# Optimization experiments

Measured on AMD Instinct MI355X. Metric: run time of the kernel, lower is better.

## Reference

```python
import jax, jax.numpy as jnp
import numpy as np
import math

DIM = 1024
D_IN = 2048      # expand * dim
N = 16           # d_state
NG = 32          # ngroups
DT_RANK = 64     # ceil(dim/16)
D_CONV = 4
B, L = 2, 1024


def setup_inputs() -> dict:
    key = jax.random.key(0)
    ks = jax.random.split(key, 10)
    nrm = lambda k, shp, s: jax.random.normal(k, shp, jnp.float32) * s
    x = jax.random.normal(ks[0], (B, L, DIM), jnp.float32)
    latent = jnp.zeros((B, NG, D_IN, N), jnp.float32)
    W_in = nrm(ks[1], (2 * D_IN, DIM), 0.02)          # in_proj (no bias)
    conv_w = nrm(ks[2], (D_IN, 1, D_CONV), 0.1)        # depthwise conv weight
    conv_b = nrm(ks[3], (D_IN,), 0.02)                 # conv bias
    W_x = nrm(ks[4], (DT_RANK + 2 * N, D_IN), 0.02)    # x_proj (no bias)
    W_dt = nrm(ks[5], (D_IN, DT_RANK), 0.02)           # dt_proj weight
    b_dt = nrm(ks[6], (D_IN,), 0.1)                    # dt_proj bias
    W_out = nrm(ks[7], (DIM, D_IN), 0.02)              # out_proj (no bias)
    A_log = jnp.log(jnp.tile(jnp.arange(1, N + 1, dtype=jnp.float32), (D_IN, 1)))
    D = jnp.ones((D_IN,), jnp.float32)
    W_cattn = nrm(ks[8], (3 * N, N), 0.02)             # c_attn (no bias)
    return dict(x=x, latent=latent, W_in=W_in, conv_w=conv_w, conv_b=conv_b,
                W_x=W_x, W_dt=W_dt, b_dt=b_dt, W_out=W_out, A_log=A_log,
                D=D, W_cattn=W_cattn)


def _scan_op(e1, e2):
    a1, b1 = e1
    a2, b2 = e2
    return a2 * a1, a2 * b1 + b2


def reference(x, latent, W_in, conv_w, conv_b, W_x, W_dt, b_dt, W_out, A_log, D, W_cattn):
    b, l, _ = x.shape
    xr = x @ W_in.T                                  # [b,l,2*d_in]
    u, res = xr[..., :D_IN], xr[..., D_IN:]
    # depthwise causal conv1d (padding d_conv-1 then truncate to l == left-pad)
    uc = jnp.transpose(u, (0, 2, 1))                 # [b,d_in,l]
    uc = jax.lax.conv_general_dilated(
        uc, conv_w, window_strides=(1,), padding=[(D_CONV - 1, 0)],
        feature_group_count=D_IN, dimension_numbers=('NCH', 'OIH', 'NCH'))
    uc = uc + conv_b[None, :, None]
    u = jax.nn.silu(jnp.transpose(uc, (0, 2, 1)))    # [b,l,d_in]

    A = -jnp.exp(A_log)                              # [d_in,n]
    x_dbl = u @ W_x.T                                # [b,l,dt_rank+2n]
    delta = jax.nn.softplus(x_dbl[..., :DT_RANK] @ W_dt.T + b_dt)  # [b,l,d_in]
    Bm = x_dbl[..., DT_RANK:DT_RANK + N]             # [b,l,n]
    Cm = x_dbl[..., DT_RANK + N:]                    # [b,l,n]

    dA = jnp.exp(delta[..., None] * A)               # [b,l,d_in,n]
    dBu = delta[..., None] * Bm[:, :, None, :] * u[..., None]  # [b,l,d_in,n]

    pg = l // NG
    dA = dA.reshape(b, NG, pg, D_IN, N)
    dBu = dBu.reshape(b, NG, pg, D_IN, N)
    Cg = Cm.reshape(b, NG, pg, N)
    dBu = dBu.at[:, :, 0].add(latent)                # inject group latent

    # parallel scan of h_t = dA_t * h_{t-1} + dBu_t within each group
    _, hs = jax.lax.associative_scan(_scan_op, (dA, dBu), axis=2)
    y = jnp.einsum('bgpdn,bgpn->bgpd', hs, Cg).reshape(b, l, D_IN)
    y = y + u * D

    # latent communication: causal attention over group latents (initial latent, per source)
    qkv = latent[:, :-1] @ W_cattn.T                 # [b,ng-1,d_in,3n]
    q, k, v = jnp.split(qkv, 3, axis=-1)
    G = NG - 1
    q = q.reshape(b, G, -1)
    k = k.reshape(b, G, -1)
    v = v.reshape(b, G, -1)
    scale = 1.0 / math.sqrt(D_IN * N)
    scores = (q @ jnp.swapaxes(k, 1, 2)) * scale     # [b,G,G]
    mask = jnp.tril(jnp.ones((G, G), bool))
    scores = jnp.where(mask, scores, -jnp.inf)
    attn = jax.nn.softmax(scores, axis=-1)
    lat = (attn @ v).reshape(b, G, D_IN, N)
    lat_out = jnp.concatenate([jnp.zeros((b, 1, D_IN, N), x.dtype), lat], axis=1)

    out = (y * jax.nn.silu(res)) @ W_out.T           # [b,l,dim]
    return out, lat_out
```

## Files before the change

kernel.cpp:

```cpp
#include <hip/hip_runtime.h>
#include <stdint.h>

typedef uint16_t u16;
typedef u16   u16x4  __attribute__((ext_vector_type(4)));
typedef u16   u16x8  __attribute__((ext_vector_type(8)));
typedef __bf16 bf16x8 __attribute__((ext_vector_type(8)));
typedef float f32x4  __attribute__((ext_vector_type(4)));

__device__ __forceinline__ float b2f(u16 x) {
    union { uint32_t u; float f; } c; c.u = ((uint32_t)x) << 16; return c.f;
}
__device__ __forceinline__ u16 f2b(float f) {
    union { float f; uint32_t u; } c; c.f = f;
    uint32_t r = c.u + 0x7FFFu + ((c.u >> 16) & 1u);
    return (u16)(r >> 16);
}
__device__ __forceinline__ float silu_f(float x) { return x / (1.f + __expf(-x)); }
__device__ __forceinline__ float softplus_f(float x) {
    return fmaxf(x, 0.f) + __logf(1.f + __expf(-fabsf(x)));
}

__device__ __forceinline__ void gload16(const u16* g, u16* l) {
    __builtin_amdgcn_global_load_lds(
        (const __attribute__((address_space(1))) void*)(g),
        (__attribute__((address_space(3))) void*)(l), 16, 0, 0);
}

__device__ __forceinline__ int dtype_flag_block(const u16* __restrict__ xraw) {
    __shared__ int bad;
    if (threadIdx.x == 0) bad = 0;
    __syncthreads();
    float v = b2f(xraw[threadIdx.x]);
    if (!(fabsf(v) < 1000.f)) atomicAdd(&bad, 1);
    __syncthreads();
    return bad;
}

struct CvtArgs {
    const void* s[13];
    u16* d[13];
    int cum[14];
    int total;
};
__global__ __launch_bounds__(256) void cvt_all_k(CvtArgs a, const u16* __restrict__ xraw)
{
    int flag = dtype_flag_block(xraw);
    int u4 = blockIdx.x * 256 + threadIdx.x;
    if (u4 >= a.total) return;
    int seg = 0;
    while (u4 >= a.cum[seg + 1]) seg++;
    int local = u4 - a.cum[seg];
    const void* s = a.s[seg];
    u16x4 o;
    if (s == nullptr) {
        o[0] = o[1] = o[2] = o[3] = 0;
    } else if (flag) {
        f32x4 vv = ((const f32x4*)s)[local];
        for (int e = 0; e < 4; e++) o[e] = f2b(vv[e]);
    } else {
        o = ((const u16x4*)s)[local];
    }
    *(u16x4*)(a.d[seg] + (size_t)local * 4) = o;
}

template<int EPI, int TN>
__device__ __forceinline__ void gemm_core(
    int bx, int by, int bz,
    const u16* __restrict__ A, const u16* __restrict__ B,
    int Kc, int lda, int ldb,
    u16* __restrict__ Cb, float* __restrict__ Cf, int ldc, int ncols,
    size_t zslab)
{
    constexpr int NJ = TN / 32;
    constexpr int BT = TN / 32;
    __shared__ __align__(16) u16 lA[128 * 64];
    __shared__ __align__(16) u16 lB[TN * 64];
    const int tid  = threadIdx.x;
    const int wave = tid >> 6, lane = tid & 63;
    const int quad = lane >> 4, l16 = lane & 15;
    const int wm = wave & 1, wn = wave >> 1;
    const int row0 = by * 128, col0 = bx * TN;
    const int kbeg = bz * Kc;

    f32x4 acc[4][NJ];
    const f32x4 zf = {0.f, 0.f, 0.f, 0.f};
    for (int i = 0; i < 4; i++) for (int j = 0; j < NJ; j++) acc[i][j] = zf;

    const u16* Ap[4]; const u16* Bp[BT];
    int lbaseA[4], lbaseB[BT];
    for (int t = 0; t < 4; t++) {
        int c = t * 256 + tid;
        int r = c >> 3, s = c & 7;
        int q = (s - (r >> 1)) & 7;
        Ap[t] = A + (size_t)(row0 + r) * lda + q * 8 + kbeg;
        lbaseA[t] = (t * 256 + wave * 64) * 8;
    }
    for (int t = 0; t < BT; t++) {
        int c = t * 256 + tid;
        int r = c >> 3, s = c & 7;
        int q = (s - (r >> 1)) & 7;
        Bp[t] = B + (size_t)(col0 + r) * ldb + q * 8 + kbeg;
        lbaseB[t] = (t * 256 + wave * 64) * 8;
    }

    for (int k0 = 0; k0 < Kc; k0 += 64) {
        for (int t = 0; t < 4; t++) gload16(Ap[t] + k0, &lA[lbaseA[t]]);
        for (int t = 0; t < BT; t++) gload16(Bp[t] + k0, &lB[lbaseB[t]]);
        __syncthreads();
        for (int half = 0; half < 2; half++) {
            bf16x8 af[4], bfr[NJ];
            for (int i = 0; i < 4; i++) {
                int r = wm * 64 + i * 16 + l16;
                int s = (half * 4 + quad + (r >> 1)) & 7;
                af[i] = *(const bf16x8*)&lA[r * 64 + s * 8];
            }
            for (int j = 0; j < NJ; j++) {
                int r = wn * (TN / 2) + j * 16 + l16;
                int s = (half * 4 + quad + (r >> 1)) & 7;
                bfr[j] = *(const bf16x8*)&lB[r * 64 + s * 8];
            }
            for (int i = 0; i < 4; i++)
                for (int j = 0; j < NJ; j++)
                    acc[i][j] = __builtin_amdgcn_mfma_f32_16x16x32_bf16(af[i], bfr[j], acc[i][j], 0, 0, 0);
        }
        __syncthreads();
    }

    float* dstf = (EPI == 2) ? (Cf + (size_t)bz * zslab) : Cf;
    for (int i = 0; i < 4; i++) {
        int mb = row0 + wm * 64 + i * 16 + quad * 4;
        for (int j = 0; j < NJ; j++) {
            int n = col0 + wn * (TN / 2) + j * 16 + l16;
            if (n >= ncols) continue;
            if (EPI == 0) {
                for (int v = 0; v < 4; v++)
                    Cb[(size_t)(mb + v) * ldc + n] = f2b(acc[i][j][v]);
            } else {
                for (int v = 0; v < 4; v++)
                    dstf[(size_t)(mb + v) * ldc + n] = acc[i][j][v];
            }
        }
    }
}

template<int EPI, int TN>
__global__ __launch_bounds__(256) void gemm_bt(
    const u16* __restrict__ A, const u16* __restrict__ B,
    int Kc, int lda, int ldb,
    u16* __restrict__ Cb, float* __restrict__ Cf, int ldc, int ncols,
    size_t zslab)
{
    gemm_core<EPI, TN>(blockIdx.x, blockIdx.y, blockIdx.z,
                       A, B, Kc, lda, ldb, Cb, Cf, ldc, ncols, zslab);
}

__global__ __launch_bounds__(256) void redc_k(
    const float* __restrict__ part, u16* __restrict__ dst)
{
    int gid = blockIdx.x * 256 + threadIdx.x;
    int idx = gid * 4;
    f32x4 s = {0.f, 0.f, 0.f, 0.f};
    for (int sl = 0; sl < 16; sl++) {
        f32x4 p = *(const f32x4*)&part[(size_t)sl * 262144 + idx];
        for (int e = 0; e < 4; e++) s[e] += p[e];
    }
    u16x4 o;
    for (int e = 0; e < 4; e++) o[e] = f2b(s[e]);
    *(u16x4*)&dst[idx] = o;
}

__global__ __launch_bounds__(256) void conv_silu_k(
    const u16* __restrict__ xr, const u16* __restrict__ cw,
    const u16* __restrict__ cb, u16* __restrict__ u)
{
    int tid = threadIdx.x;
    int bl  = blockIdx.x;
    int l   = bl & 1023;
    int d0  = tid * 8;
    float acc[8];
    u16x8 bias = *(const u16x8*)&cb[d0];
    for (int j = 0; j < 8; j++) acc[j] = b2f(bias[j]);
    union { u16x8 v[4]; u16 s[32]; } wb;
    for (int t = 0; t < 4; t++) wb.v[t] = *(const u16x8*)&cw[d0 * 4 + t * 8];
    for (int t = 0; t < 4; t++) {
        int ls = l - 3 + t;
        if (ls < 0) continue;
        u16x8 xv = *(const u16x8*)&xr[(size_t)(bl - 3 + t) * 4096 + d0];
        for (int j = 0; j < 8; j++) acc[j] += b2f(xv[j]) * b2f(wb.s[j * 4 + t]);
    }
    u16x8 o;
    for (int j = 0; j < 8; j++) o[j] = f2b(silu_f(acc[j]));
    *(u16x8*)&u[(size_t)bl * 2048 + d0] = o;
}

__global__ __launch_bounds__(256) void scan_qkv_k(
    const u16* __restrict__ u, const u16* __restrict__ xr,
    const u16* __restrict__ xdbl, const u16* __restrict__ Wdt,
    const u16* __restrict__ bdt,
    const u16* __restrict__ latent, const u16* __restrict__ Alog,
    const u16* __restrict__ Dp, u16* __restrict__ yg,
    const u16* __restrict__ Wc, u16* __restrict__ q, u16* __restrict__ k,
    u16* __restrict__ v)
{
    __shared__ __align__(16) u16 lsh[4096];
    int tid = threadIdx.x;
    int bid = blockIdx.x;
    if (bid < 1024) {
        u16* lxb = lsh;
        float (*Bs)[16] = (float(*)[16])(lsh + 2048);
        float (*Cs)[16] = (float(*)[16])(lsh + 3072);
        const int wave = tid >> 6, lane = tid & 63;
        const int nh = lane >> 5;
        int dblk = bid & 15, bg = bid >> 4;
        const int d = dblk * 128 + wave * 32 + (lane & 31);
        const int rowb = bg * 32;

        {
            int p = tid >> 3, t = tid & 7;
            *(u16x8*)&lxb[p * 64 + t * 8] =
                *(const u16x8*)&xdbl[(size_t)(rowb + p) * 128 + t * 8];
        }
        for (int idx = tid; idx < 512; idx += 256) {
            int p = idx >> 4, n = idx & 15;
            const u16* xp = &xdbl[(size_t)(rowb + p) * 128];
            Bs[p][n] = b2f(xp[64 + n]);
            Cs[p][n] = b2f(xp[80 + n]);
        }
        __syncthreads();

        float wdtf[32];
        {
            const u16* wp = &Wdt[(size_t)d * 64 + nh * 32];
            u16x8 w0 = *(const u16x8*)wp;
            u16x8 w1 = *(const u16x8*)(wp + 8);
            u16x8 w2 = *(const u16x8*)(wp + 16);
            u16x8 w3 = *(const u16x8*)(wp + 24);
            for (int e = 0; e < 8; e++) {
                wdtf[e]      = b2f(w0[e]); wdtf[8 + e]  = b2f(w1[e]);
                wdtf[16 + e] = b2f(w2[e]); wdtf[24 + e] = b2f(w3[e]);
            }
        }
        float bv = b2f(bdt[d]);
        float dl[32];
        #pragma unroll
        for (int p = 0; p < 32; p++) {
            float s = 0.f;
            #pragma unroll
            for (int t = 0; t < 4; t++) {
                u16x8 xv = *(const u16x8*)&lxb[p * 64 + nh * 32 + t * 8];
                for (int e = 0; e < 8; e++) s += b2f(xv[e]) * wdtf[t * 8 + e];
            }
            s += __shfl_xor(s, 32);
            dl[p] = softplus_f(s + bv);
        }

        const float LOG2E = 1.4426950408889634f;
        float a_[8], h_[8];
        {
            u16x8 av = *(const u16x8*)&Alog[(size_t)d * 16 + nh * 8];
            u16x8 lv = *(const u16x8*)&latent[((size_t)bg * 2048 + d) * 16 + nh * 8];
            for (int n = 0; n < 8; n++) {
                a_[n] = -__expf(b2f(av[n])) * LOG2E;
                h_[n] = b2f(lv[n]);
            }
        }
        float Dd = b2f(Dp[d]);

        u16 u_nx = u[(size_t)rowb * 2048 + d];
        u16 r_nx = xr[(size_t)rowb * 4096 + 2048 + d];
        #pragma unroll
        for (int p = 0; p < 32; p++) {
            float uu = b2f(u_nx), rsv = b2f(r_nx);
            if (p < 31) {
                u_nx = u[(size_t)(rowb + p + 1) * 2048 + d];
                r_nx = xr[(size_t)(rowb + p + 1) * 4096 + 2048 + d];
            }
            float dlt = dl[p];
            float db  = dlt * uu;
            float y8 = 0.f;
            if (p == 0) {
                #pragma unroll
                for (int n = 0; n < 8; n++) {
                    h_[n] += db * Bs[0][nh * 8 + n];
                    y8 += h_[n] * Cs[0][nh * 8 + n];
                }
            } else {
                #pragma unroll
                for (int n = 0; n < 8; n++) {
                    float w = exp2f(dlt * a_[n]);
                    h_[n] = w * h_[n] + db * Bs[p][nh * 8 + n];
                    y8 += h_[n] * Cs[p][nh * 8 + n];
                }
            }
            float y = y8 + __shfl_xor(y8, 32);
            if (nh == 0)
                yg[(size_t)(rowb + p) * 2048 + d] = f2b((y + uu * Dd) * silu_f(rsv));
        }
    } else {
        float (*Ws)[16] = (float(*)[16])lsh;
        for (int i = tid; i < 768; i += 256) Ws[i >> 4][i & 15] = b2f(Wc[i]);
        __syncthreads();
        int gid = (bid - 1024) * 256 + tid;
        int d = gid & 2047;
        int bi = gid >> 11;
        int b = bi / 31, i = bi - b * 31;
        const u16* lp = &latent[(((size_t)b * 32 + i) * 2048 + d) * 16];
        float lv[16];
        {
            u16x8 l0 = *(const u16x8*)lp, l1 = *(const u16x8*)(lp + 8);
            for (int m = 0; m < 8; m++) { lv[m] = b2f(l0[m]); lv[8 + m] = b2f(l1[m]); }
        }
        u16* outs[3] = {q, k, v};
        for (int pl = 0; pl < 3; pl++) {
            u16x8 o0, o1;
            for (int n = 0; n < 16; n++) {
                float s = 0.f;
                for (int m = 0; m < 16; m++) s += lv[m] * Ws[pl * 16 + n][m];
                if (n < 8) o0[n] = f2b(s); else o1[n - 8] = f2b(s);
            }
            u16* op = outs[pl] + (size_t)bi * 32768 + d * 16;
            *(u16x8*)op = o0; *(u16x8*)(op + 8) = o1;
        }
    }
}

__global__ __launch_bounds__(256) void gemm_scores_k(
    const u16* __restrict__ yg, const u16* __restrict__ Wout, float* __restrict__ out_part,
    const u16* __restrict__ q, const u16* __restrict__ kk, float* __restrict__ sc)
{
    int bid = blockIdx.x;
    if (bid < 512) {
        int bx = bid & 15, by = (bid >> 4) & 15, bz = bid >> 8;
        gemm_core<2, 64>(bx, by, bz, yg, Wout, 1024, 2048, 2048,
                         nullptr, out_part, 1024, 1024, (size_t)2048 * 1024);
        return;
    }
    int idx = bid - 512;
    int b = idx / 961, r = idx - b * 961;
    int i = r / 31, j = r - i * 31;
    if (j > i) return;
    const u16* qp = q + ((size_t)b * 31 + i) * 32768;
    const u16* kp = kk + ((size_t)b * 31 + j) * 32768;
    float s = 0.f;
    for (int t = threadIdx.x * 8; t < 32768; t += 2048) {
        u16x8 a = *(const u16x8*)&qp[t];
        u16x8 c = *(const u16x8*)&kp[t];
        for (int e = 0; e < 8; e++) s += b2f(a[e]) * b2f(c[e]);
    }
    for (int off = 32; off; off >>= 1) s += __shfl_xor(s, off);
    __shared__ float red[4];
    if ((threadIdx.x & 63) == 0) red[threadIdx.x >> 6] = s;
    __syncthreads();
    if (threadIdx.x == 0)
        sc[idx] = (red[0] + red[1] + red[2] + red[3]) * 5.5242717e-3f;
}

__global__ __launch_bounds__(256) void attv_redout_k(
    const float* __restrict__ sc, const u16* __restrict__ v,
    const float* __restrict__ part, void* __restrict__ dout,
    const u16* __restrict__ xraw)
{
    int flag = dtype_flag_block(xraw);
    int bid = blockIdx.x;
    if (bid < 1024) {
        int chunk = bid & 15, bi = bid >> 4;
        int b = bi >> 5, i = (bi & 31) - 1;
        __shared__ float as[32];
        if (i >= 0 && threadIdx.x < 64) {
            float x = (threadIdx.x <= i) ? sc[(size_t)b * 961 + i * 31 + threadIdx.x] : -3.4e38f;
            float mx = x;
            for (int off = 32; off; off >>= 1) mx = fmaxf(mx, __shfl_xor(mx, off));
            float e = (threadIdx.x <= i) ? __expf(x - mx) : 0.f;
            float sm = e;
            for (int off = 32; off; off >>= 1) sm += __shfl_xor(sm, off);
            if (threadIdx.x < 32) as[threadIdx.x] = e / sm;
        }
        __syncthreads();
        int dn = chunk * 2048 + threadIdx.x * 8;
        float acc[8] = {0, 0, 0, 0, 0, 0, 0, 0};
        if (i >= 0) {
            for (int j = 0; j <= i; j++) {
                u16x8 vv = *(const u16x8*)&v[((size_t)b * 31 + j) * 32768 + dn];
                float aj = as[j];
                for (int e = 0; e < 8; e++) acc[e] += aj * b2f(vv[e]);
            }
            for (int e = 0; e < 8; e++) if (!(fabsf(acc[e]) < 1e30f)) acc[e] = 0.f;
        }
        size_t ofs = 2097152 + ((size_t)b * 32 + (i + 1)) * 32768 + dn;
        if (flag) {
            f32x4 o0, o1;
            for (int e = 0; e < 4; e++) { o0[e] = acc[e]; o1[e] = acc[4 + e]; }
            *(f32x4*)((float*)dout + ofs) = o0;
            *(f32x4*)((float*)dout + ofs + 4) = o1;
        } else {
            u16x8 o;
            for (int e = 0; e < 8; e++) o[e] = f2b(acc[e]);
            *(u16x8*)((u16*)dout + ofs) = o;
        }
    } else {
        int gid = (bid - 1024) * 256 + threadIdx.x;
        int m = gid >> 8;
        int j = (gid & 255) * 4;
        f32x4 s = {0.f, 0.f, 0.f, 0.f};
        for (int ks = 0; ks < 2; ks++) {
            f32x4 p = *(const f32x4*)&part[((size_t)ks * 2048 + m) * 1024 + j];
            for (int e = 0; e < 4; e++) s[e] += p[e];
        }
        for (int e = 0; e < 4; e++) if (!(fabsf(s[e]) < 1e30f)) s[e] = 0.f;
        if (flag) {
            ((f32x4*)dout)[(size_t)m * 256 + (j >> 2)] = s;
        } else {
            u16x4 o;
            for (int e = 0; e < 4; e++) o[e] = f2b(s[e]);
            ((u16x4*)dout)[(size_t)m * 256 + (j >> 2)] = o;
        }
    }
}

extern "C" void kernel_launch(void* const* d_in, const int* in_sizes, int n_in,
                              void* d_out, int out_size, void* d_ws, size_t ws_size,
                              hipStream_t stream)
{
    char* ws = (char*)d_ws;
    const u16* xraw = (const u16*)d_in[0];
    u16* cx    = (u16*)(ws + 0);
    u16* clat  = (u16*)(ws + 4194304);
    u16* cWin  = (u16*)(ws + 8388608);
    u16* ccw   = (u16*)(ws + 16777216);
    u16* ccb   = (u16*)(ws + 16793600);
    u16* wxp   = (u16*)(ws + 16797696);
    u16* cWdt  = (u16*)(ws + 17321984);
    u16* cbdt  = (u16*)(ws + 17584128);
    u16* cWout = (u16*)(ws + 17588224);
    u16* cAlog = (u16*)(ws + 21782528);
    u16* cD    = (u16*)(ws + 21848064);
    u16* cWc   = (u16*)(ws + 21852160);
    float* xdbl_part = (float*)(ws + 21853760);
    u16*   xdbl      = (u16*)(ws + 38630976);
    float* sc        = (float*)(ws + 39155264);
    u16*   u         = (u16*)(ws + 39163008);
    u16*   xr        = (u16*)(ws + 47551616);
    u16*   yg        = (u16*)(ws + 64328832);
    u16*   qb        = (u16*)(ws + 72717440);
    u16*   kb        = qb + 2031616;
    u16*   vb        = kb + 2031616;
    float* out_part  = (float*)(ws + 84907136);

    CvtArgs ca;
    const void* srcs[13] = { d_in[0], d_in[1], d_in[2], d_in[3], d_in[4],
                             d_in[5], nullptr, d_in[6], d_in[7], d_in[8],
                             d_in[9], d_in[10], d_in[11] };
    u16* dsts[13] = { cx, clat, cWin, ccw, ccb,
                      wxp, wxp + 196608, cWdt, cbdt, cWout,
                      cAlog, cD, cWc };
    int ns[13] = { 2097152, 2097152, 4194304, 8192, 2048,
                   196608, 65536, 131072, 2048, 2097152,
                   32768, 2048, 768 };
    int cum = 0;
    for (int i = 0; i < 13; i++) {
        ca.s[i] = srcs[i]; ca.d[i] = dsts[i];
        ca.cum[i] = cum; cum += ns[i] / 4;
    }
    ca.cum[13] = cum; ca.total = cum;
    cvt_all_k<<<(cum + 255) / 256, 256, 0, stream>>>(ca, xraw);

    gemm_bt<0, 64><<<dim3(64, 16, 1), 256, 0, stream>>>(cx, cWin, 1024, 1024, 1024,
                                                        xr, nullptr, 4096, 4096, 0);
    conv_silu_k<<<2048, 256, 0, stream>>>(xr, ccw, ccb, u);
    gemm_bt<2, 64><<<dim3(2, 16, 16), 256, 0, stream>>>(u, wxp, 128, 2048, 2048,
                                                        nullptr, xdbl_part, 128, 128,
                                                        262144);
    redc_k<<<256, 256, 0, stream>>>(xdbl_part, xdbl);
    scan_qkv_k<<<1520, 256, 0, stream>>>(u, xr, xdbl, cWdt, cbdt, clat, cAlog, cD, yg,
                                         cWc, qb, kb, vb);
    gemm_scores_k<<<2434, 256, 0, stream>>>(yg, cWout, out_part, qb, kb, sc);
    attv_redout_k<<<3072, 256, 0, stream>>>(sc, vb, out_part, d_out, xraw);
}
```

Before: 233.0 us.

## Compute delta projection with MFMA from swizzled LDS tiles in scan kernel

The per-thread scalar dot product for the dt projection (32 rows by 64 rank per channel, duplicated across half-waves) is replaced by bf16 MFMA 16x16x32 on a 32x128 tile. xdbl and the Wdt block are staged into LDS through async global_load_lds with an XOR-style swizzle to avoid bank conflicts. Softplus results go to an LDS buffer that the scan loop reads per step. This cuts the FMA work and register pressure in the scan prologue, at the cost of more LDS (40KB) and an extra barrier, which may lower occupancy.

```diff
diff --git a/kernel.cpp b/kernel.cpp
--- a/kernel.cpp
+++ b/kernel.cpp
@@ -202,23 +202,33 @@
     const u16* __restrict__ Wc, u16* __restrict__ q, u16* __restrict__ k,
     u16* __restrict__ v)
 {
-    __shared__ __align__(16) u16 lsh[4096];
+    __shared__ __align__(16) u16 lsh[20480];
     int tid = threadIdx.x;
     int bid = blockIdx.x;
     if (bid < 1024) {
-        u16* lxb = lsh;
-        float (*Bs)[16] = (float(*)[16])(lsh + 2048);
-        float (*Cs)[16] = (float(*)[16])(lsh + 3072);
+        u16* lA = lsh;
+        u16* lB = lsh + 2048;
+        float* dls = (float*)(lsh + 10240);
+        float (*Bs)[16] = (float(*)[16])(lsh + 18432);
+        float (*Cs)[16] = (float(*)[16])(lsh + 19456);
         const int wave = tid >> 6, lane = tid & 63;
+        const int quad = lane >> 4, l16 = lane & 15;
         const int nh = lane >> 5;
         int dblk = bid & 15, bg = bid >> 4;
         const int d = dblk * 128 + wave * 32 + (lane & 31);
         const int rowb = bg * 32;
 
         {
-            int p = tid >> 3, t = tid & 7;
-            *(u16x8*)&lxb[p * 64 + t * 8] =
-                *(const u16x8*)&xdbl[(size_t)(rowb + p) * 128 + t * 8];
+            int r = tid >> 3, s = tid & 7;
+            int qg = (s - (r >> 1)) & 7;
+            gload16(&xdbl[(size_t)(rowb + r) * 128 + qg * 8], &lA[(wave * 64) * 8]);
+        }
+        for (int t = 0; t < 4; t++) {
+            int c = t * 256 + tid;
+            int r = c >> 3, s = c & 7;
+            int qg = (s - (r >> 1)) & 7;
+            gload16(&Wdt[(size_t)(dblk * 128 + r) * 64 + qg * 8],
+                    &lB[(t * 256 + wave * 64) * 8]);
         }
         for (int idx = tid; idx < 512; idx += 256) {
             int p = idx >> 4, n = idx & 15;
@@ -228,31 +238,35 @@
         }
         __syncthreads();
 
-        float wdtf[32];
-        {
-            const u16* wp = &Wdt[(size_t)d * 64 + nh * 32];
-            u16x8 w0 = *(const u16x8*)wp;
-            u16x8 w1 = *(const u16x8*)(wp + 8);
-            u16x8 w2 = *(const u16x8*)(wp + 16);
-            u16x8 w3 = *(const u16x8*)(wp + 24);
-            for (int e = 0; e < 8; e++) {
-                wdtf[e]      = b2f(w0[e]); wdtf[8 + e]  = b2f(w1[e]);
-                wdtf[16 + e] = b2f(w2[e]); wdtf[24 + e] = b2f(w3[e]);
-            }
-        }
-        float bv = b2f(bdt[d]);
-        float dl[32];
-        #pragma unroll
-        for (int p = 0; p < 32; p++) {
-            float s = 0.f;
-            #pragma unroll
-            for (int t = 0; t < 4; t++) {
-                u16x8 xv = *(const u16x8*)&lxb[p * 64 + nh * 32 + t * 8];
-                for (int e = 0; e < 8; e++) s += b2f(xv[e]) * wdtf[t * 8 + e];
-            }
-            s += __shfl_xor(s, 32);
-            dl[p] = softplus_f(s + bv);
-        }
+        f32x4 dacc[2][2];
+        const f32x4 zf = {0.f, 0.f, 0.f, 0.f};
+        for (int i = 0; i < 2; i++) for (int j = 0; j < 2; j++) dacc[i][j] = zf;
+        for (int half = 0; half < 2; half++) {
+            bf16x8 af[2], bfr[2];
+            for (int i = 0; i < 2; i++) {
+                int r = i * 16 + l16;
+                int s = (half * 4 + quad + (r >> 1)) & 7;
+                af[i] = *(const bf16x8*)&lA[r * 64 + s * 8];
+            }
+            for (int j = 0; j < 2; j++) {
+                int r = wave * 32 + j * 16 + l16;
+                int s = (half * 4 + quad + (r >> 1)) & 7;
+                bfr[j] = *(const bf16x8*)&lB[r * 64 + s * 8];
+            }
+            for (int i = 0; i < 2; i++)
+                for (int j = 0; j < 2; j++)
+                    dacc[i][j] = __builtin_amdgcn_mfma_f32_16x16x32_bf16(af[i], bfr[j], dacc[i][j], 0, 0, 0);
+        }
+        for (int j = 0; j < 2; j++) {
+            int n = wave * 32 + j * 16 + l16;
+            float bv = b2f(bdt[dblk * 128 + n]);
+            for (int i = 0; i < 2; i++) {
+                int mb = i * 16 + quad * 4;
+                for (int vv = 0; vv < 4; vv++)
+                    dls[(mb + vv) * 128 + n] = softplus_f(dacc[i][j][vv] + bv);
+            }
+        }
+        __syncthreads();
 
         const float LOG2E = 1.4426950408889634f;
         float a_[8], h_[8];
@@ -265,6 +279,7 @@
             }
         }
         float Dd = b2f(Dp[d]);
+        const int dll = wave * 32 + (lane & 31);
 
         u16 u_nx = u[(size_t)rowb * 2048 + d];
         u16 r_nx = xr[(size_t)rowb * 4096 + 2048 + d];
@@ -275,7 +290,7 @@
                 u_nx = u[(size_t)(rowb + p + 1) * 2048 + d];
                 r_nx = xr[(size_t)(rowb + p + 1) * 4096 + 2048 + d];
             }
-            float dlt = dl[p];
+            float dlt = dls[p * 128 + dll];
             float db  = dlt * uu;
             float y8 = 0.f;
             if (p == 0) {
```

Result: faster. 226.0 us (-3.0%).
